# Performance work log

Hardware: AMD Instinct MI355X
Metric: run time of the kernel (lower is better)

The kernel has to match this reference:

```python
import jax, jax.numpy as jnp
import numpy as np

N, D, N_CLASSES = 8192, 512, 128
POS_MARGIN = 1.0  # default path: sample_method=None, Dynamic_margin=None


def setup_inputs() -> dict:
    key = jax.random.key(0)
    k1, k2 = jax.random.split(key)
    x = jax.random.normal(k1, (N, D), dtype=jnp.float32)
    # metric-learning embeddings are L2-normalized so sim in [-1, 1]
    x = x / jnp.linalg.norm(x, axis=1, keepdims=True)
    targets = jax.random.randint(k2, (N,), 0, N_CLASSES, dtype=jnp.int64)
    return {"inputs": x, "targets": targets, "nonorm": 0}


def reference(inputs, targets, nonorm):
    n = inputs.shape[0]
    sim = jnp.matmul(inputs, inputs.T)                      # [n, n]
    same = targets[:, None] == targets[None, :]             # [n, n]
    pos_mask = same & (sim < POS_MARGIN)                    # drops self-sim == 1
    neg_mask = ~same

    # per-row masked log-sum-exp (sort in original is irrelevant to the sums)
    pos_sum = jnp.sum(jnp.where(pos_mask, jnp.exp(1.0 - sim), 0.0), axis=1)
    neg_sum = jnp.sum(jnp.where(neg_mask, jnp.exp(sim), 0.0), axis=1)
    pos_loss = jnp.log(pos_sum)
    neg_loss = jnp.log(neg_sum)

    has_neg = jnp.any(neg_mask, axis=1)                     # rows w/o negs are skipped
    loss = jnp.sum(jnp.where(has_neg, pos_loss + neg_loss, 0.0)) / n
    prec = jnp.mean(1.0 - has_neg.astype(jnp.float32))      # fraction of skipped rows

    # torch code reports means of the LAST row's pos/neg pairs
    last_pos = pos_mask[-1]
    last_neg = neg_mask[-1]
    mean_pos_sim = jnp.sum(jnp.where(last_pos, sim[-1], 0.0)) / jnp.sum(last_pos)
    mean_neg_sim = jnp.sum(jnp.where(last_neg, sim[-1], 0.0)) / jnp.sum(last_neg)
    return loss, prec, mean_pos_sim, mean_neg_sim
```

## Files before the change

### kernel.cpp

```cpp
#include <hip/hip_runtime.h>
#include <math.h>

#define N_ 8192
#define D_ 512
#define NC_ 128
#define T_ 64

typedef __attribute__((ext_vector_type(8))) short bf16x8;
typedef __attribute__((ext_vector_type(4))) float f32x4;
typedef __attribute__((ext_vector_type(4))) unsigned short us4;

static __device__ __forceinline__ unsigned short f2bf(float f) {
    union { float f; unsigned u; } c; c.f = f;
    unsigned u = c.u;
    u += 0x7fffu + ((u >> 16) & 1u);
    return (unsigned short)(u >> 16);
}

__global__ __launch_bounds__(256) void k_convert(const float* __restrict__ x,
                                                 unsigned short* __restrict__ xb) {
    int i = (blockIdx.x * 256 + threadIdx.x);
    float4 v = reinterpret_cast<const float4*>(x)[i];
    us4 o = { f2bf(v.x), f2bf(v.y), f2bf(v.z), f2bf(v.w) };
    reinterpret_cast<us4*>(xb)[i] = o;
}

__global__ __launch_bounds__(256, 4) void k_main(const unsigned short* __restrict__ xb,
                                                 const int* __restrict__ tg,
                                                 float* __restrict__ bufP,
                                                 float* __restrict__ bufN) {
    __shared__ alignas(16) unsigned short As[128 * 64];
    __shared__ alignas(16) unsigned short Bs[128 * 64];
    __shared__ int rowT[128];

    const int tid  = threadIdx.x;
    const int w    = tid >> 6;
    const int lane = tid & 63;
    const int q    = lane >> 4;
    const int l15  = lane & 15;
    const int wrow = w >> 1;
    const int wcol = w & 1;

    int rem = blockIdx.x;
    int it = 0;
    while (rem >= (T_ - it)) { rem -= (T_ - it); it++; }
    const int jt = it + rem;
    const int row0 = it * 128;
    const int col0 = jt * 128;

    if (tid < 128) rowT[tid] = tg[row0 + tid];
    __syncthreads();

    int tR[4][4];
#pragma unroll
    for (int mi = 0; mi < 4; ++mi)
#pragma unroll
        for (int r = 0; r < 4; ++r)
            tR[mi][r] = rowT[wrow * 64 + mi * 16 + q * 4 + r];

    int tC[4];
#pragma unroll
    for (int ni = 0; ni < 4; ++ni)
        tC[ni] = tg[col0 + wcol * 64 + ni * 16 + l15];

    f32x4 acc[4][4];
#pragma unroll
    for (int mi = 0; mi < 4; ++mi)
#pragma unroll
        for (int ni = 0; ni < 4; ++ni)
            acc[mi][ni] = (f32x4){0.f, 0.f, 0.f, 0.f};

    for (int ks = 0; ks < 8; ++ks) {
        const int k0 = ks * 64;
        __syncthreads();
#pragma unroll
        for (int itr = 0; itr < 4; ++itr) {
            int gs = (itr * 4 + w) * 64 + lane;
            int r  = gs >> 3;
            int s  = gs & 7;
            int g  = s ^ (r & 7);
            const unsigned short* ga = xb + (size_t)(row0 + r) * D_ + k0 + g * 8;
            const unsigned short* gb = xb + (size_t)(col0 + r) * D_ + k0 + g * 8;
            __builtin_amdgcn_global_load_lds(
                (const __attribute__((address_space(1))) void*)ga,
                (__attribute__((address_space(3))) void*)(As + (itr * 4 + w) * 512),
                16, 0, 0);
            __builtin_amdgcn_global_load_lds(
                (const __attribute__((address_space(1))) void*)gb,
                (__attribute__((address_space(3))) void*)(Bs + (itr * 4 + w) * 512),
                16, 0, 0);
        }
        __syncthreads();

#pragma unroll
        for (int kc = 0; kc < 2; ++kc) {
            bf16x8 aF[4], bF[4];
#pragma unroll
            for (int mi = 0; mi < 4; ++mi) {
                int rA = wrow * 64 + mi * 16 + l15;
                int g  = kc * 4 + q;
                int s  = g ^ (rA & 7);
                aF[mi] = *reinterpret_cast<const bf16x8*>(As + rA * 64 + s * 8);
            }
#pragma unroll
            for (int ni = 0; ni < 4; ++ni) {
                int rB = wcol * 64 + ni * 16 + l15;
                int g  = kc * 4 + q;
                int s  = g ^ (rB & 7);
                bF[ni] = *reinterpret_cast<const bf16x8*>(Bs + rB * 64 + s * 8);
            }
#pragma unroll
            for (int mi = 0; mi < 4; ++mi)
#pragma unroll
                for (int ni = 0; ni < 4; ++ni)
                    acc[mi][ni] = __builtin_amdgcn_mfma_f32_16x16x32_bf16(
                        aF[mi], bF[ni], acc[mi][ni], 0, 0, 0);
        }
    }

    float ps[4][4], ns[4][4];
    float cps[4], cns[4];
#pragma unroll
    for (int mi = 0; mi < 4; ++mi)
#pragma unroll
        for (int r = 0; r < 4; ++r) { ps[mi][r] = 0.f; ns[mi][r] = 0.f; }
#pragma unroll
    for (int ni = 0; ni < 4; ++ni) { cps[ni] = 0.f; cns[ni] = 0.f; }

#pragma unroll
    for (int mi = 0; mi < 4; ++mi)
#pragma unroll
        for (int ni = 0; ni < 4; ++ni)
#pragma unroll
            for (int r = 0; r < 4; ++r) {
                float s = acc[mi][ni][r];
                bool same = (tR[mi][r] == tC[ni]);
                float e = __expf(same ? 1.0f - s : s);
                float pe = (same && (s < 1.0f)) ? e : 0.0f;
                float ne = same ? 0.0f : e;
                ps[mi][r] += pe; ns[mi][r] += ne;
                cps[ni]   += pe; cns[ni]   += ne;
            }

    __syncthreads();
    float* scr = (float*)As;

#pragma unroll
    for (int mi = 0; mi < 4; ++mi)
#pragma unroll
        for (int r = 0; r < 4; ++r) {
            float p = ps[mi][r];
            float n = ns[mi][r];
#pragma unroll
            for (int m = 1; m < 16; m <<= 1) {
                p += __shfl_xor(p, m, 64);
                n += __shfl_xor(n, m, 64);
            }
            if (l15 == 0) {
                int rloc = wrow * 64 + mi * 16 + q * 4 + r;
                scr[wcol * 128 + rloc]       = p;
                scr[256 + wcol * 128 + rloc] = n;
            }
        }

#pragma unroll
    for (int ni = 0; ni < 4; ++ni) {
        float p = cps[ni];
        float n = cns[ni];
        p += __shfl_xor(p, 16, 64); p += __shfl_xor(p, 32, 64);
        n += __shfl_xor(n, 16, 64); n += __shfl_xor(n, 32, 64);
        if (q == 0) {
            int cloc = wcol * 64 + ni * 16 + l15;
            scr[512 + wrow * 128 + cloc] = p;
            scr[768 + wrow * 128 + cloc] = n;
        }
    }
    __syncthreads();

    if (tid < 128) {
        int r = tid;
        size_t off = ((size_t)it * T_ + jt) * 128 + r;
        bufP[off] = scr[r]       + scr[128 + r];
        bufN[off] = scr[256 + r] + scr[384 + r];
    } else if (jt != it) {
        int c = tid - 128;
        size_t off = ((size_t)jt * T_ + it) * 128 + c;
        bufP[off] = scr[512 + c] + scr[640 + c];
        bufN[off] = scr[768 + c] + scr[896 + c];
    }
}

__global__ __launch_bounds__(256) void k_last(const float* __restrict__ x,
                                              double* __restrict__ sim_last) {
    int j    = (blockIdx.x * 256 + threadIdx.x) >> 6;
    int lane = threadIdx.x & 63;
    const float* xl = x + (size_t)(N_ - 1) * D_;
    const float* xj = x + (size_t)j * D_;
    double acc = 0.0;
#pragma unroll
    for (int it = 0; it < 8; ++it) {
        int k = it * 64 + lane;
        acc += (double)xl[k] * (double)xj[k];
    }
#pragma unroll
    for (int m = 32; m >= 1; m >>= 1) acc += __shfl_xor(acc, m, 64);
    if (lane == 0) sim_last[j] = acc;
}

__global__ __launch_bounds__(256) void k_reduce(const float* __restrict__ bufP,
                                                const float* __restrict__ bufN,
                                                float* __restrict__ psum,
                                                float* __restrict__ nsum) {
    int t    = blockIdx.x;
    int half = threadIdx.x >> 7;
    int r    = threadIdx.x & 127;
    const float* buf = half ? bufN : bufP;
    const float* base = buf + (size_t)t * T_ * 128 + r;
    float s = 0.f;
#pragma unroll
    for (int o = 0; o < T_; ++o) s += base[o * 128];
    if (half) nsum[t * 128 + r] = s;
    else      psum[t * 128 + r] = s;
}

__global__ __launch_bounds__(1024) void k_final(const float* __restrict__ psum,
                                                const float* __restrict__ nsum,
                                                const int* __restrict__ tg,
                                                const double* __restrict__ sim_last,
                                                float* __restrict__ out) {
    __shared__ int lh[NC_];
    __shared__ double sl[1024], sp[1024], sn[1024];
    __shared__ int    sk[1024], cp[1024], cn[1024];
    int tid = threadIdx.x;

    if (tid < NC_) lh[tid] = 0;
    __syncthreads();
    for (int i = tid; i < N_; i += 1024) atomicAdd(&lh[tg[i]], 1);
    __syncthreads();

    double part = 0.0;
    int skip = 0;
    for (int i = tid; i < N_; i += 1024) {
        if (lh[tg[i]] < N_) {
            part += (double)(logf(psum[i]) + logf(nsum[i]));
        } else {
            skip++;
        }
    }

    double pd = 0.0, nd = 0.0;
    int pc = 0, nc = 0;
    int tlast = tg[N_ - 1];
    for (int j = tid; j < N_; j += 1024) {
        double s = sim_last[j];
        if (tg[j] == tlast) {
            if (s < 1.0) { pd += s; pc++; }
        } else {
            nd += s; nc++;
        }
    }

    sl[tid] = part; sk[tid] = skip;
    sp[tid] = pd;   cp[tid] = pc;
    sn[tid] = nd;   cn[tid] = nc;
    __syncthreads();
    for (int s = 512; s >= 1; s >>= 1) {
        if (tid < s) {
            sl[tid] += sl[tid + s]; sk[tid] += sk[tid + s];
            sp[tid] += sp[tid + s]; cp[tid] += cp[tid + s];
            sn[tid] += sn[tid + s]; cn[tid] += cn[tid + s];
        }
        __syncthreads();
    }
    if (tid == 0) {
        out[0] = (float)(sl[0] / (double)N_);
        out[1] = (float)sk[0] / (float)N_;
        out[2] = (float)(sp[0] / (double)cp[0]);
        out[3] = (float)(sn[0] / (double)cn[0]);
    }
}

extern "C" void kernel_launch(void* const* d_in, const int* in_sizes, int n_in,
                              void* d_out, int out_size, void* d_ws, size_t ws_size,
                              hipStream_t stream) {
    const float* x  = (const float*)d_in[0];
    const int*   tg = (const int*)d_in[1];
    char* ws = (char*)d_ws;

    unsigned short* xb = (unsigned short*)ws;
    const size_t XB = (size_t)N_ * D_ * 2;
    float*  psum     = (float*)(ws + XB);
    float*  nsum     = (float*)(ws + XB + 32768);
    double* sim_last = (double*)(ws + XB + 65536);
    float*  bufP     = (float*)(ws + XB + 131072);
    float*  bufN     = (float*)(ws + XB + 131072 + 2097152);

    const int nblk_tri = T_ * (T_ + 1) / 2;

    hipLaunchKernelGGL(k_convert, dim3((N_ * D_) / (256 * 4)), dim3(256), 0, stream, x, xb);
    hipLaunchKernelGGL(k_main, dim3(nblk_tri), dim3(256), 0, stream, xb, tg, bufP, bufN);
    hipLaunchKernelGGL(k_last, dim3((N_ * 64) / 256), dim3(256), 0, stream, x, sim_last);
    hipLaunchKernelGGL(k_reduce, dim3(T_), dim3(256), 0, stream, bufP, bufN, psum, nsum);
    hipLaunchKernelGGL(k_final, dim3(1), dim3(1024), 0, stream,
                       psum, nsum, tg, sim_last, (float*)d_out);
}
```

Baseline: 166.1 us.

## Widen symmetric Gram tiles to 128x256 with 512-thread blocks

The main kernel now computes a 128x256 output tile per block with 8 waves instead of 128x128 with 4 waves. It re-enumerates the upper-triangle blocks at half-column granularity, masks out sub-tiles below the diagonal, and changes the partial-sum buffer indexing and the reduce loop bounds to match. Each block reuses its A tile across twice as many columns, which cuts global and LDS traffic for A and reduces block count. In exchange it computes some redundant sub-tiles on the diagonal, uses more LDS per block, and may lower occupancy.

Result: no change. 167.0 us (+0.5%).

```diff
diff --git a/kernel.cpp b/kernel.cpp
--- a/kernel.cpp
+++ b/kernel.cpp
@@ -25,12 +25,12 @@
     reinterpret_cast<us4*>(xb)[i] = o;
 }
 
-__global__ __launch_bounds__(256, 4) void k_main(const unsigned short* __restrict__ xb,
+__global__ __launch_bounds__(512, 4) void k_main(const unsigned short* __restrict__ xb,
                                                  const int* __restrict__ tg,
                                                  float* __restrict__ bufP,
                                                  float* __restrict__ bufN) {
     __shared__ alignas(16) unsigned short As[128 * 64];
-    __shared__ alignas(16) unsigned short Bs[128 * 64];
+    __shared__ alignas(16) unsigned short Bs[256 * 64];
     __shared__ int rowT[128];
 
     const int tid  = threadIdx.x;
@@ -38,15 +38,18 @@
     const int lane = tid & 63;
     const int q    = lane >> 4;
     const int l15  = lane & 15;
-    const int wrow = w >> 1;
-    const int wcol = w & 1;
+    const int wrow = w >> 2;
+    const int wcol = w & 3;
 
     int rem = blockIdx.x;
     int it = 0;
-    while (rem >= (T_ - it)) { rem -= (T_ - it); it++; }
-    const int jt = it + rem;
+    while (rem >= 32 - (it >> 1)) { rem -= 32 - (it >> 1); it++; }
+    const int jt2  = (it >> 1) + rem;
     const int row0 = it * 128;
-    const int col0 = jt * 128;
+    const int col0 = jt2 * 256;
+
+    const int bsub   = 2 * jt2 + (wcol >> 1);
+    const bool rowOK = (bsub >= it);
 
     if (tid < 128) rowT[tid] = tg[row0 + tid];
     __syncthreads();
@@ -74,20 +77,27 @@
         const int k0 = ks * 64;
         __syncthreads();
 #pragma unroll
-        for (int itr = 0; itr < 4; ++itr) {
-            int gs = (itr * 4 + w) * 64 + lane;
-            int r  = gs >> 3;
-            int s  = gs & 7;
+        for (int i2 = 0; i2 < 2; ++i2) {
+            int slot = i2 * 512 + tid;
+            int r  = slot >> 3;
+            int s  = slot & 7;
             int g  = s ^ (r & 7);
             const unsigned short* ga = xb + (size_t)(row0 + r) * D_ + k0 + g * 8;
+            __builtin_amdgcn_global_load_lds(
+                (const __attribute__((address_space(1))) void*)ga,
+                (__attribute__((address_space(3))) void*)(As + (i2 * 512 + w * 64) * 8),
+                16, 0, 0);
+        }
+#pragma unroll
+        for (int i2 = 0; i2 < 4; ++i2) {
+            int slot = i2 * 512 + tid;
+            int r  = slot >> 3;
+            int s  = slot & 7;
+            int g  = s ^ (r & 7);
             const unsigned short* gb = xb + (size_t)(col0 + r) * D_ + k0 + g * 8;
             __builtin_amdgcn_global_load_lds(
-                (const __attribute__((address_space(1))) void*)ga,
-                (__attribute__((address_space(3))) void*)(As + (itr * 4 + w) * 512),
-                16, 0, 0);
-            __builtin_amdgcn_global_load_lds(
                 (const __attribute__((address_space(1))) void*)gb,
-                (__attribute__((address_space(3))) void*)(Bs + (itr * 4 + w) * 512),
+                (__attribute__((address_space(3))) void*)(Bs + (i2 * 512 + w * 64) * 8),
                 16, 0, 0);
         }
         __syncthreads();
@@ -127,20 +137,22 @@
 #pragma unroll
     for (int ni = 0; ni < 4; ++ni) { cps[ni] = 0.f; cns[ni] = 0.f; }
 
-#pragma unroll
-    for (int mi = 0; mi < 4; ++mi)
-#pragma unroll
-        for (int ni = 0; ni < 4; ++ni)
-#pragma unroll
-            for (int r = 0; r < 4; ++r) {
-                float s = acc[mi][ni][r];
-                bool same = (tR[mi][r] == tC[ni]);
-                float e = __expf(same ? 1.0f - s : s);
-                float pe = (same && (s < 1.0f)) ? e : 0.0f;
-                float ne = same ? 0.0f : e;
-                ps[mi][r] += pe; ns[mi][r] += ne;
-                cps[ni]   += pe; cns[ni]   += ne;
-            }
+    if (rowOK) {
+#pragma unroll
+        for (int mi = 0; mi < 4; ++mi)
+#pragma unroll
+            for (int ni = 0; ni < 4; ++ni)
+#pragma unroll
+                for (int r = 0; r < 4; ++r) {
+                    float s = acc[mi][ni][r];
+                    bool same = (tR[mi][r] == tC[ni]);
+                    float e = __expf(same ? 1.0f - s : s);
+                    float pe = (same && (s < 1.0f)) ? e : 0.0f;
+                    float ne = same ? 0.0f : e;
+                    ps[mi][r] += pe; ns[mi][r] += ne;
+                    cps[ni]   += pe; cns[ni]   += ne;
+                }
+    }
 
     __syncthreads();
     float* scr = (float*)As;
@@ -159,7 +171,7 @@
             if (l15 == 0) {
                 int rloc = wrow * 64 + mi * 16 + q * 4 + r;
                 scr[wcol * 128 + rloc]       = p;
-                scr[256 + wcol * 128 + rloc] = n;
+                scr[512 + wcol * 128 + rloc] = n;
             }
         }
 
@@ -171,22 +183,26 @@
         n += __shfl_xor(n, 16, 64); n += __shfl_xor(n, 32, 64);
         if (q == 0) {
             int cloc = wcol * 64 + ni * 16 + l15;
-            scr[512 + wrow * 128 + cloc] = p;
-            scr[768 + wrow * 128 + cloc] = n;
+            scr[1024 + wrow * 256 + cloc] = p;
+            scr[1536 + wrow * 256 + cloc] = n;
         }
     }
     __syncthreads();
 
     if (tid < 128) {
         int r = tid;
-        size_t off = ((size_t)it * T_ + jt) * 128 + r;
-        bufP[off] = scr[r]       + scr[128 + r];
-        bufN[off] = scr[256 + r] + scr[384 + r];
-    } else if (jt != it) {
-        int c = tid - 128;
-        size_t off = ((size_t)jt * T_ + it) * 128 + c;
-        bufP[off] = scr[512 + c] + scr[640 + c];
-        bufN[off] = scr[768 + c] + scr[896 + c];
+        int s_row = it + jt2 - (it >> 1);
+        size_t off = ((size_t)it * T_ + s_row) * 128 + r;
+        bufP[off] = scr[r] + scr[128 + r] + scr[256 + r] + scr[384 + r];
+        bufN[off] = scr[512 + r] + scr[640 + r] + scr[768 + r] + scr[896 + r];
+    } else if (tid < 384) {
+        int c  = tid - 128;
+        int bc = 2 * jt2 + (c >> 7);
+        if (bc > it) {
+            size_t off = ((size_t)bc * T_ + it) * 128 + (c & 127);
+            bufP[off] = scr[1024 + c] + scr[1280 + c];
+            bufN[off] = scr[1536 + c] + scr[1792 + c];
+        }
     }
 }
 
@@ -214,11 +230,11 @@
     int t    = blockIdx.x;
     int half = threadIdx.x >> 7;
     int r    = threadIdx.x & 127;
+    int smax = t + 32 - (t >> 1);
     const float* buf = half ? bufN : bufP;
     const float* base = buf + (size_t)t * T_ * 128 + r;
     float s = 0.f;
-#pragma unroll
-    for (int o = 0; o < T_; ++o) s += base[o * 128];
+    for (int o = 0; o < smax; ++o) s += base[o * 128];
     if (half) nsum[t * 128 + r] = s;
     else      psum[t * 128 + r] = s;
 }
@@ -295,10 +311,10 @@
     float*  bufP     = (float*)(ws + XB + 131072);
     float*  bufN     = (float*)(ws + XB + 131072 + 2097152);
 
-    const int nblk_tri = T_ * (T_ + 1) / 2;
+    const int nblk = 1056;
 
     hipLaunchKernelGGL(k_convert, dim3((N_ * D_) / (256 * 4)), dim3(256), 0, stream, x, xb);
-    hipLaunchKernelGGL(k_main, dim3(nblk_tri), dim3(256), 0, stream, xb, tg, bufP, bufN);
+    hipLaunchKernelGGL(k_main, dim3(nblk), dim3(512), 0, stream, xb, tg, bufP, bufN);
     hipLaunchKernelGGL(k_last, dim3((N_ * 64) / 256), dim3(256), 0, stream, x, sim_last);
     hipLaunchKernelGGL(k_reduce, dim3(T_), dim3(256), 0, stream, bufP, bufN, psum, nsum);
     hipLaunchKernelGGL(k_final, dim3(1), dim3(1024), 0, stream,
```
